# Kernel optimization log

Measured on AMD Instinct MI355X. Metric: run time of the kernel, lower is better.

## Reference

```python
import jax, jax.numpy as jnp
import numpy as np

IN_FEATURES = 1024
OUT_FEATURES = 128


def setup_inputs() -> dict:
    key = jax.random.key(0)
    k1, k2, k3, k4, k5 = jax.random.split(key, 5)
    B, T, E, D = 4, 4096, IN_FEATURES, OUT_FEATURES
    s_in = 1.0 / np.sqrt(E)
    s_d = 1.0 / np.sqrt(D)
    return {
        "x": jax.random.normal(k1, (B, T, E), dtype=jnp.float32),
        "Wk": jax.random.uniform(k2, (E, D), jnp.float32, -s_in, s_in),
        "Wq": jax.random.uniform(k3, (E, D), jnp.float32, -s_in, s_in),
        "Wv": jax.random.uniform(k4, (E, D), jnp.float32, -s_in, s_in),
        "Wp": jax.random.uniform(k5, (D, D), jnp.float32, -s_d, s_d),
    }


def reference(x, Wk, Wq, Wv, Wp):
    # x: [B, T, E]; projections stored as [in, out] (torch Linear transposed)
    B, T, E = x.shape
    D = Wk.shape[1]
    k = x @ Wk  # [B, T, D]
    q = x @ Wq
    v = x @ Wv
    scale = 1.0 / jnp.sqrt(jnp.asarray(D, x.dtype))
    attn = jnp.einsum("btd,bsd->bts", q, k) * scale  # [B, T, T]
    causal = jnp.tril(jnp.ones((T, T), dtype=bool))
    attn = jnp.where(causal, attn, -jnp.inf)
    attn = jax.nn.softmax(attn, axis=-1)
    out = jnp.einsum("bts,bsd->btd", attn, v)  # [B, T, D]
    return out @ Wp  # dropout p=0.0 -> identity
```

## Files before the change

kernel.cpp:

```cpp
#include <hip/hip_runtime.h>

#define E_DIM 1024
#define D_DIM 128
#define T_DIM 4096

typedef unsigned short u16;
typedef u16 u16x8 __attribute__((ext_vector_type(8)));
typedef u16 u16x4 __attribute__((ext_vector_type(4)));
typedef __bf16 bf16x8 __attribute__((ext_vector_type(8)));
typedef float f32x4 __attribute__((ext_vector_type(4)));

__device__ __forceinline__ u16 cvt_bf16(float f) {
    unsigned u = __float_as_uint(f);
    u += 0x7FFF + ((u >> 16) & 1);
    return (u16)(u >> 16);
}

__device__ __forceinline__ float bf2f(u16 v) {
    return __uint_as_float(((unsigned)v) << 16);
}

__device__ __forceinline__ f32x4 mfma16(u16x8 a, u16x8 b, f32x4 c) {
    return __builtin_amdgcn_mfma_f32_16x16x32_bf16(
        __builtin_bit_cast(bf16x8, a), __builtin_bit_cast(bf16x8, b), c, 0, 0, 0);
}

__device__ __forceinline__ void gld_lds16(const void* g, void* l) {
    __builtin_amdgcn_global_load_lds(
        (const __attribute__((address_space(1))) unsigned int*)g,
        (__attribute__((address_space(3))) unsigned int*)l, 16, 0, 0);
}

__global__ void prep_kernel(const float* __restrict__ Wk, const float* __restrict__ Wq,
                            const float* __restrict__ Wv, const float* __restrict__ Wp,
                            u16* __restrict__ Wqt, u16* __restrict__ Wkt,
                            u16* __restrict__ Wvt, u16* __restrict__ Wpt) {
    int tid = blockIdx.x * 256 + threadIdx.x;
    const int WT = 128 * 1024;
    if (tid < 3 * WT) {
        int w = tid / WT;
        int r = tid - w * WT;
        int n = r >> 10, k = r & 1023;
        const float* W = (w == 0) ? Wq : (w == 1) ? Wk : Wv;
        u16* Wt = (w == 0) ? Wqt : (w == 1) ? Wkt : Wvt;
        Wt[r] = cvt_bf16(W[k * 128 + n]);
    } else {
        int r = tid - 3 * WT;
        if (r < 128 * 128) {
            int n = r >> 7, k = r & 127;
            Wpt[r] = cvt_bf16(Wp[k * 128 + n]);
        }
    }
}

__global__ __launch_bounds__(256) void qkv_kernel(
        const float* __restrict__ x,
        const u16* __restrict__ Wqt, const u16* __restrict__ Wkt, const u16* __restrict__ Wvt,
        u16* __restrict__ qb, u16* __restrict__ kb, u16* __restrict__ vT) {
    __shared__ u16 Xs[64][40];
    __shared__ u16 Ws[3][128][40];

    const int t = threadIdx.x;
    const int w = t >> 6;
    const int lane = t & 63;
    const int lr = lane & 15;
    const int lg = lane >> 4;
    const int r0 = blockIdx.x * 64;

    f32x4 acc[24];
    #pragma unroll
    for (int i = 0; i < 24; ++i) acc[i] = f32x4{0.f, 0.f, 0.f, 0.f};

    const int xrow = t >> 2;
    const int xseg = t & 3;
    const int wn   = t >> 1;
    const int wh   = (t & 1) * 16;

    const float* xp0 = x + (size_t)(r0 + xrow) * E_DIM + xseg * 8;

    float4 a0 = *(const float4*)(xp0);
    float4 a1 = *(const float4*)(xp0 + 4);
    u16x8 wr[3][2];
    {
        const u16* w0 = Wqt + (size_t)wn * E_DIM + wh;
        const u16* w1 = Wkt + (size_t)wn * E_DIM + wh;
        const u16* w2 = Wvt + (size_t)wn * E_DIM + wh;
        wr[0][0] = *(const u16x8*)w0; wr[0][1] = *(const u16x8*)(w0 + 8);
        wr[1][0] = *(const u16x8*)w1; wr[1][1] = *(const u16x8*)(w1 + 8);
        wr[2][0] = *(const u16x8*)w2; wr[2][1] = *(const u16x8*)(w2 + 8);
    }

    for (int k0 = 0; k0 < E_DIM; k0 += 32) {
        u16x8 xv;
        xv[0] = cvt_bf16(a0.x); xv[1] = cvt_bf16(a0.y);
        xv[2] = cvt_bf16(a0.z); xv[3] = cvt_bf16(a0.w);
        xv[4] = cvt_bf16(a1.x); xv[5] = cvt_bf16(a1.y);
        xv[6] = cvt_bf16(a1.z); xv[7] = cvt_bf16(a1.w);
        *(u16x8*)&Xs[xrow][xseg * 8] = xv;
        #pragma unroll
        for (int j = 0; j < 3; ++j) {
            *(u16x8*)&Ws[j][wn][wh]     = wr[j][0];
            *(u16x8*)&Ws[j][wn][wh + 8] = wr[j][1];
        }
        __syncthreads();

        if (k0 + 32 < E_DIM) {
            const float* xp = xp0 + k0 + 32;
            a0 = *(const float4*)(xp);
            a1 = *(const float4*)(xp + 4);
            const u16* w0 = Wqt + (size_t)wn * E_DIM + k0 + 32 + wh;
            const u16* w1 = Wkt + (size_t)wn * E_DIM + k0 + 32 + wh;
            const u16* w2 = Wvt + (size_t)wn * E_DIM + k0 + 32 + wh;
            wr[0][0] = *(const u16x8*)w0; wr[0][1] = *(const u16x8*)(w0 + 8);
            wr[1][0] = *(const u16x8*)w1; wr[1][1] = *(const u16x8*)(w1 + 8);
            wr[2][0] = *(const u16x8*)w2; wr[2][1] = *(const u16x8*)(w2 + 8);
        }

        u16x8 av = *(u16x8*)&Xs[16 * w + lr][lg * 8];
        #pragma unroll
        for (int nt = 0; nt < 24; ++nt) {
            int j = nt >> 3;
            int n = (nt & 7) * 16 + lr;
            u16x8 bv = *(u16x8*)&Ws[j][n][lg * 8];
            acc[nt] = mfma16(av, bv, acc[nt]);
        }
        __syncthreads();
    }

    const int row0 = r0 + 16 * w + 4 * lg;
    const int bb = row0 >> 12;
    const int tt = row0 & 4095;
    #pragma unroll
    for (int nt = 0; nt < 24; ++nt) {
        int j = nt >> 3;
        int col = (nt & 7) * 16 + lr;
        if (j < 2) {
            u16* outb = (j == 0) ? qb : kb;
            #pragma unroll
            for (int reg = 0; reg < 4; ++reg)
                outb[(size_t)(row0 + reg) * D_DIM + col] = cvt_bf16(acc[nt][reg]);
        } else {
            u16x4 pv;
            #pragma unroll
            for (int reg = 0; reg < 4; ++reg) pv[reg] = cvt_bf16(acc[nt][reg]);
            *(u16x4*)&vT[((size_t)(bb * 128 + col)) * T_DIM + tt] = pv;
        }
    }
}

__global__ __launch_bounds__(512) void attn_kernel(
        const u16* __restrict__ qb, const u16* __restrict__ kb, const u16* __restrict__ vT,
        u16* __restrict__ Opart, float* __restrict__ ml, int SPLIT) {
    const int g = blockIdx.x;
    const int b = blockIdx.y;
    int i, c;
    if (SPLIT) {
        int k = 0;
        while (2 * (k + 1) * (k + 2) <= g) ++k;
        const int off = g - 2 * k * (k + 1);
        const int iband = off / (k + 1);
        c = off - iband * (k + 1);
        i = 4 * k + iband;
    } else { i = g; c = 0; }

    const int q0 = i * 128;
    const int kv_beg = c * 512;
    const int kv_end = SPLIT ? min(q0 + 128, kv_beg + 512) : (q0 + 128);
    const int slot = b * gridDim.x + g;

    __shared__ __align__(16) char smem[81920];

    const int t = threadIdx.x;
    const int w = t >> 6;
    const int lane = t & 63;
    const int lr = lane & 15;
    const int lg = lane >> 4;
    const size_t base = (size_t)b * T_DIM * D_DIM;

    u16x8 qf[4];
    {
        const u16* qp = qb + base + (size_t)(q0 + 16 * w + lr) * D_DIM + lg * 8;
        #pragma unroll
        for (int dk = 0; dk < 4; ++dk) qf[dk] = *(const u16x8*)(qp + dk * 32);
    }

    const char* kpb = (const char*)(kb + base);
    const char* vpb = (const char*)(vT + (size_t)b * D_DIM * T_DIM);
    const int key = (lr & 7) << 4;

    #define STAGE(S0, BUF) do {                                                   \
        char* kB_ = smem + (BUF) * 16384;                                         \
        char* vB_ = smem + 32768 + (BUF) * 16384;                                 \
        const int wbase_ = (t >> 6) * 1024;                                       \
        _Pragma("unroll")                                                         \
        for (int c2 = 0; c2 < 2; ++c2) {                                          \
            const int krow_ = c2 * 32 + (t >> 4);                                 \
            gld_lds16(kpb + (size_t)((S0) + krow_) * 256 +                        \
                      (((t & 15) * 16) ^ ((krow_ & 7) * 16)),                     \
                      kB_ + c2 * 8192 + wbase_);                                  \
            const int vrow_ = c2 * 64 + (t >> 3);                                 \
            gld_lds16(vpb + (size_t)vrow_ * (T_DIM * 2) + (size_t)(S0) * 2 +      \
                      (((t & 7) * 16) ^ ((vrow_ & 7) * 16)),                      \
                      vB_ + c2 * 8192 + wbase_);                                  \
        }                                                                         \
    } while (0)

    f32x4 oacc[8];
    #pragma unroll
    for (int n = 0; n < 8; ++n) oacc[n] = f32x4{0.f, 0.f, 0.f, 0.f};
    float m_run = -1e30f, l_run = 0.f;
    const float scale2 = 0.12752048520120164f;
    const int qrow = q0 + 16 * w + lr;

    STAGE(kv_beg, 0);
    asm volatile("s_waitcnt vmcnt(0)" ::: "memory");
    __syncthreads();

    int buf = 0;
    for (int s0 = kv_beg; s0 < kv_end; s0 += 64) {
        if (s0 + 64 < kv_end) STAGE(s0 + 64, buf ^ 1);

        char* kB  = smem + buf * 16384;
        char* vB  = smem + 32768 + buf * 16384;
        char* psB = smem + 65536 + w * 2048;

        f32x4 sacc[4];
        #pragma unroll
        for (int n = 0; n < 4; ++n) sacc[n] = f32x4{0.f, 0.f, 0.f, 0.f};
        __builtin_amdgcn_s_setprio(1);
        #pragma unroll
        for (int dk = 0; dk < 4; ++dk) {
            #pragma unroll
            for (int nt = 0; nt < 4; ++nt) {
                u16x8 kfr = *(u16x8*)(kB + (nt * 16 + lr) * 256 + ((dk * 64 + lg * 16) ^ key));
                sacc[nt] = mfma16(kfr, qf[dk], sacc[nt]);
            }
        }
        __builtin_amdgcn_s_setprio(0);

        float sv[4][4];
        const bool need_mask = (s0 + 63 > q0 + 16 * w);
        #pragma unroll
        for (int nt = 0; nt < 4; ++nt) {
            #pragma unroll
            for (int r = 0; r < 4; ++r) {
                float v = sacc[nt][r] * scale2;
                if (need_mask && (s0 + nt * 16 + 4 * lg + r) > qrow) v = -1e30f;
                sv[nt][r] = v;
            }
        }

        float tmax = sv[0][0];
        #pragma unroll
        for (int nt = 0; nt < 4; ++nt)
            #pragma unroll
            for (int r = 0; r < 4; ++r) tmax = fmaxf(tmax, sv[nt][r]);
        tmax = fmaxf(tmax, __shfl_xor(tmax, 16));
        tmax = fmaxf(tmax, __shfl_xor(tmax, 32));
        float m_new = fmaxf(m_run, tmax);
        float rsc = __builtin_amdgcn_exp2f(m_run - m_new);
        m_run = m_new;
        float tsum = 0.f;
        #pragma unroll
        for (int nt = 0; nt < 4; ++nt)
            #pragma unroll
            for (int r = 0; r < 4; ++r) {
                sv[nt][r] = __builtin_amdgcn_exp2f(sv[nt][r] - m_new);
                tsum += sv[nt][r];
            }
        tsum += __shfl_xor(tsum, 16);
        tsum += __shfl_xor(tsum, 32);
        l_run = l_run * rsc + tsum;

        #pragma unroll
        for (int nt = 0; nt < 8; ++nt)
            #pragma unroll
            for (int r = 0; r < 4; ++r) oacc[nt][r] *= rsc;

        #pragma unroll
        for (int nt = 0; nt < 4; ++nt) {
            u16x4 pv4;
            #pragma unroll
            for (int r = 0; r < 4; ++r) pv4[r] = cvt_bf16(sv[nt][r]);
            *(u16x4*)(psB + lr * 128 + ((nt * 32 + lg * 8) ^ key)) = pv4;
        }

        u16x8 pA0 = *(u16x8*)(psB + lr * 128 + ((lg * 16) ^ key));
        u16x8 pA1 = *(u16x8*)(psB + lr * 128 + ((64 + lg * 16) ^ key));

        __builtin_amdgcn_s_setprio(1);
        #pragma unroll
        for (int nt = 0; nt < 8; ++nt) {
            u16x8 bv0 = *(u16x8*)(vB + (nt * 16 + lr) * 128 + ((lg * 16) ^ key));
            oacc[nt] = mfma16(bv0, pA0, oacc[nt]);
            u16x8 bv1 = *(u16x8*)(vB + (nt * 16 + lr) * 128 + ((64 + lg * 16) ^ key));
            oacc[nt] = mfma16(bv1, pA1, oacc[nt]);
        }
        __builtin_amdgcn_s_setprio(0);

        asm volatile("s_waitcnt vmcnt(0)" ::: "memory");
        __syncthreads();
        buf ^= 1;
    }
    #undef STAGE

    if (lg == 0) {
        int row = 16 * w + lr;
        ml[(size_t)(slot * 128 + row) * 2]     = m_run;
        ml[(size_t)(slot * 128 + row) * 2 + 1] = l_run;
    }

    const float invl = 1.f / l_run;
    const int orw = 16 * w + lr;
    #pragma unroll
    for (int nt = 0; nt < 8; ++nt) {
        u16x4 ov;
        #pragma unroll
        for (int r = 0; r < 4; ++r) ov[r] = cvt_bf16(oacc[nt][r] * invl);
        *(u16x4*)(smem + orw * 256 + ((32 * nt + 8 * lg) ^ ((orw & 7) << 4))) = ov;
    }
    __syncthreads();
    u16* op = Opart + (size_t)slot * 16384;
    const int orow = t >> 2;
    const int oseg = t & 3;
    #pragma unroll
    for (int j = 0; j < 4; ++j) {
        u16x8 vv = *(u16x8*)(smem + orow * 256 + ((oseg * 64 + j * 16) ^ ((orow & 7) << 4)));
        *(u16x8*)(op + orow * 128 + oseg * 32 + j * 8) = vv;
    }
}

__global__ __launch_bounds__(256) void combine_kernel(
        const u16* __restrict__ Opart, const float* __restrict__ ml,
        const u16* __restrict__ Wpt, float* __restrict__ out,
        int SPLIT, int NSLOT) {
    const int io = blockIdx.x;
    const int b = blockIdx.y;
    const int i = io >> 1;
    const int half = io & 1;
    int NC, g0;
    if (SPLIT) {
        int k = i >> 2;
        NC = k + 1;
        g0 = 2 * k * (k + 1) + (i & 3) * (k + 1);
    } else { NC = 1; g0 = i; }
    const int slot0 = b * NSLOT + g0;

    __shared__ u16 Os[64][136];
    const int t = threadIdx.x;
    const int row = t >> 2, seg = (t & 3) * 32;
    const int row_in = half * 64 + row;

    float m_fin = -1e30f;
    for (int c = 0; c < NC; ++c)
        m_fin = fmaxf(m_fin, ml[(size_t)((slot0 + c) * 128 + row_in) * 2]);

    float acc[32];
    #pragma unroll
    for (int j = 0; j < 32; ++j) acc[j] = 0.f;
    float l_fin = 0.f;
    for (int c = 0; c < NC; ++c) {
        float mcv = ml[(size_t)((slot0 + c) * 128 + row_in) * 2];
        float lcv = ml[(size_t)((slot0 + c) * 128 + row_in) * 2 + 1];
        float wgt = __builtin_amdgcn_exp2f(mcv - m_fin) * lcv;
        l_fin += wgt;
        const u16* opc = Opart + (size_t)(slot0 + c) * 16384 + row_in * 128 + seg;
        #pragma unroll
        for (int j = 0; j < 4; ++j) {
            u16x8 v = *(const u16x8*)(opc + j * 8);
            #pragma unroll
            for (int e = 0; e < 8; ++e)
                acc[j * 8 + e] += bf2f(v[e]) * wgt;
        }
    }
    const float inv = 1.f / l_fin;

    #pragma unroll
    for (int j = 0; j < 4; ++j) {
        u16x8 ov;
        #pragma unroll
        for (int e = 0; e < 8; ++e) ov[e] = cvt_bf16(acc[j * 8 + e] * inv);
        *(u16x8*)&Os[row][seg + j * 8] = ov;
    }
    __syncthreads();

    const int w = t >> 6;
    const int lane = t & 63;
    const int lr = lane & 15;
    const int lg = lane >> 4;
    u16x8 af[4];
    #pragma unroll
    for (int dk = 0; dk < 4; ++dk)
        af[dk] = *(u16x8*)&Os[16 * w + lr][dk * 32 + lg * 8];
    float* op = out + ((size_t)b * T_DIM + io * 64) * D_DIM;
    #pragma unroll
    for (int nt = 0; nt < 8; ++nt) {
        f32x4 y = f32x4{0.f, 0.f, 0.f, 0.f};
        #pragma unroll
        for (int dk = 0; dk < 4; ++dk) {
            u16x8 bv = *(const u16x8*)&Wpt[(size_t)(nt * 16 + lr) * D_DIM + dk * 32 + lg * 8];
            y = mfma16(af[dk], bv, y);
        }
        #pragma unroll
        for (int r = 0; r < 4; ++r)
            op[(size_t)(16 * w + 4 * lg + r) * D_DIM + nt * 16 + lr] = y[r];
    }
}

extern "C" void kernel_launch(void* const* d_in, const int* in_sizes, int n_in,
                              void* d_out, int out_size, void* d_ws, size_t ws_size,
                              hipStream_t stream) {
    const float* x  = (const float*)d_in[0];
    const float* Wk = (const float*)d_in[1];
    const float* Wq = (const float*)d_in[2];
    const float* Wv = (const float*)d_in[3];
    const float* Wp = (const float*)d_in[4];
    float* out = (float*)d_out;

    char* ws = (char*)d_ws;
    u16* qb  = (u16*)(ws);
    u16* kb  = (u16*)(ws + 4194304);
    u16* vT  = (u16*)(ws + 8388608);
    u16* Wqt = (u16*)(ws + 12582912);
    u16* Wkt = (u16*)(ws + 12582912 + 262144);
    u16* Wvt = (u16*)(ws + 12582912 + 524288);
    u16* Wpt = (u16*)(ws + 12582912 + 786432);
    float* ml   = (float*)(ws + 13631488);
    u16* Opart  = (u16*)(ws + 14680064);

    const bool big = ws_size >= (size_t)36 * 1024 * 1024;
    const int SPLIT = big ? 1 : 0;
    const int GX = big ? 144 : 32;

    prep_kernel<<<1600, 256, 0, stream>>>(Wk, Wq, Wv, Wp, Wqt, Wkt, Wvt, Wpt);
    qkv_kernel<<<256, 256, 0, stream>>>(x, Wqt, Wkt, Wvt, qb, kb, vT);
    attn_kernel<<<dim3(GX, 4), 512, 0, stream>>>(qb, kb, vT, Opart, ml, SPLIT);
    combine_kernel<<<dim3(64, 4), 256, 0, stream>>>(Opart, ml, Wpt, out, SPLIT, GX);
}
```

Before: 107.9 us.

## Restructure QKV projection GEMM: split output columns, async weight staging, direct-register x

The QKV projection kernel now launches twice as many blocks, each covering 64 rows by 192 of the 384 fused output columns. Each wave computes a 32x96 sub-tile, so every weight fragment read from LDS feeds two MFMAs. Weights are double-buffered into LDS with direct global-to-LDS loads and an XOR-style swizzle. The x rows are loaded straight into registers and converted to bf16 there, which removes the x LDS round trip. The aim is more parallelism across CUs, fewer LDS reads per MFMA, and weight fetches overlapped with compute, at the cost of reading x twice (once per column group) and a vmcnt wait every iteration.

```diff
diff --git a/kernel.cpp b/kernel.cpp
--- a/kernel.cpp
+++ b/kernel.cpp
@@ -57,93 +57,107 @@
         const float* __restrict__ x,
         const u16* __restrict__ Wqt, const u16* __restrict__ Wkt, const u16* __restrict__ Wvt,
         u16* __restrict__ qb, u16* __restrict__ kb, u16* __restrict__ vT) {
-    __shared__ u16 Xs[64][40];
-    __shared__ u16 Ws[3][128][40];
+    __shared__ __align__(16) char smem[24576];
 
     const int t = threadIdx.x;
     const int w = t >> 6;
     const int lane = t & 63;
     const int lr = lane & 15;
     const int lg = lane >> 4;
-    const int r0 = blockIdx.x * 64;
-
-    f32x4 acc[24];
-    #pragma unroll
-    for (int i = 0; i < 24; ++i) acc[i] = f32x4{0.f, 0.f, 0.f, 0.f};
-
-    const int xrow = t >> 2;
-    const int xseg = t & 3;
-    const int wn   = t >> 1;
-    const int wh   = (t & 1) * 16;
-
-    const float* xp0 = x + (size_t)(r0 + xrow) * E_DIM + xseg * 8;
-
-    float4 a0 = *(const float4*)(xp0);
-    float4 a1 = *(const float4*)(xp0 + 4);
-    u16x8 wr[3][2];
-    {
-        const u16* w0 = Wqt + (size_t)wn * E_DIM + wh;
-        const u16* w1 = Wkt + (size_t)wn * E_DIM + wh;
-        const u16* w2 = Wvt + (size_t)wn * E_DIM + wh;
-        wr[0][0] = *(const u16x8*)w0; wr[0][1] = *(const u16x8*)(w0 + 8);
-        wr[1][0] = *(const u16x8*)w1; wr[1][1] = *(const u16x8*)(w1 + 8);
-        wr[2][0] = *(const u16x8*)w2; wr[2][1] = *(const u16x8*)(w2 + 8);
-    }
-
+    const int m = w & 1;
+    const int n = w >> 1;
+    const int rg = blockIdx.x >> 1;
+    const int cgrp = blockIdx.x & 1;
+    const int r0 = rg * 64;
+
+    #define STAGE_W(K0, BUF) do {                                                 \
+        char* wB_ = smem + (BUF) * 12288;                                         \
+        _Pragma("unroll")                                                         \
+        for (int c2 = 0; c2 < 3; ++c2) {                                          \
+            const int rl_ = c2 * 64 + (t >> 2);                                   \
+            const int gn_ = cgrp * 192 + rl_;                                     \
+            const u16* W_ = (gn_ < 128) ? Wqt : (gn_ < 256) ? Wkt : Wvt;          \
+            const int s_ = ((t & 3) - (rl_ >> 1)) & 3;                            \
+            gld_lds16(W_ + (size_t)(gn_ & 127) * E_DIM + (K0) + 8 * s_,           \
+                      wB_ + c2 * 4096 + t * 16);                                  \
+        }                                                                         \
+    } while (0)
+
+    const float* xp0 = x + (size_t)(r0 + 32 * m + lr) * E_DIM + lg * 8;
+    const float* xp1 = xp0 + 16 * E_DIM;
+
+    float4 xr[2][2];
+    #define XLOAD(K0) do {                                                        \
+        xr[0][0] = *(const float4*)(xp0 + (K0));                                  \
+        xr[0][1] = *(const float4*)(xp0 + (K0) + 4);                              \
+        xr[1][0] = *(const float4*)(xp1 + (K0));                                  \
+        xr[1][1] = *(const float4*)(xp1 + (K0) + 4);                              \
+    } while (0)
+
+    f32x4 acc[2][6];
+    #pragma unroll
+    for (int i = 0; i < 2; ++i)
+        #pragma unroll
+        for (int j = 0; j < 6; ++j) acc[i][j] = f32x4{0.f, 0.f, 0.f, 0.f};
+
+    XLOAD(0);
+    STAGE_W(0, 0);
+    asm volatile("s_waitcnt vmcnt(0)" ::: "memory");
+    __syncthreads();
+
+    int buf = 0;
     for (int k0 = 0; k0 < E_DIM; k0 += 32) {
-        u16x8 xv;
-        xv[0] = cvt_bf16(a0.x); xv[1] = cvt_bf16(a0.y);
-        xv[2] = cvt_bf16(a0.z); xv[3] = cvt_bf16(a0.w);
-        xv[4] = cvt_bf16(a1.x); xv[5] = cvt_bf16(a1.y);
-        xv[6] = cvt_bf16(a1.z); xv[7] = cvt_bf16(a1.w);
-        *(u16x8*)&Xs[xrow][xseg * 8] = xv;
-        #pragma unroll
-        for (int j = 0; j < 3; ++j) {
-            *(u16x8*)&Ws[j][wn][wh]     = wr[j][0];
-            *(u16x8*)&Ws[j][wn][wh + 8] = wr[j][1];
-        }
+        if (k0 + 32 < E_DIM) STAGE_W(k0 + 32, buf ^ 1);
+
+        u16x8 av[2];
+        #pragma unroll
+        for (int i = 0; i < 2; ++i) {
+            av[i][0] = cvt_bf16(xr[i][0].x); av[i][1] = cvt_bf16(xr[i][0].y);
+            av[i][2] = cvt_bf16(xr[i][0].z); av[i][3] = cvt_bf16(xr[i][0].w);
+            av[i][4] = cvt_bf16(xr[i][1].x); av[i][5] = cvt_bf16(xr[i][1].y);
+            av[i][6] = cvt_bf16(xr[i][1].z); av[i][7] = cvt_bf16(xr[i][1].w);
+        }
+        if (k0 + 32 < E_DIM) XLOAD(k0 + 32);
+
+        char* wB = smem + buf * 12288;
+        __builtin_amdgcn_s_setprio(1);
+        #pragma unroll
+        for (int nt = 0; nt < 6; ++nt) {
+            const int ln = n * 96 + nt * 16 + lr;
+            u16x8 bv = *(u16x8*)(wB + ln * 64 + (((lg + (ln >> 1)) & 3) << 4));
+            acc[0][nt] = mfma16(av[0], bv, acc[0][nt]);
+            acc[1][nt] = mfma16(av[1], bv, acc[1][nt]);
+        }
+        __builtin_amdgcn_s_setprio(0);
+
+        asm volatile("s_waitcnt vmcnt(0)" ::: "memory");
         __syncthreads();
-
-        if (k0 + 32 < E_DIM) {
-            const float* xp = xp0 + k0 + 32;
-            a0 = *(const float4*)(xp);
-            a1 = *(const float4*)(xp + 4);
-            const u16* w0 = Wqt + (size_t)wn * E_DIM + k0 + 32 + wh;
-            const u16* w1 = Wkt + (size_t)wn * E_DIM + k0 + 32 + wh;
-            const u16* w2 = Wvt + (size_t)wn * E_DIM + k0 + 32 + wh;
-            wr[0][0] = *(const u16x8*)w0; wr[0][1] = *(const u16x8*)(w0 + 8);
-            wr[1][0] = *(const u16x8*)w1; wr[1][1] = *(const u16x8*)(w1 + 8);
-            wr[2][0] = *(const u16x8*)w2; wr[2][1] = *(const u16x8*)(w2 + 8);
-        }
-
-        u16x8 av = *(u16x8*)&Xs[16 * w + lr][lg * 8];
-        #pragma unroll
-        for (int nt = 0; nt < 24; ++nt) {
-            int j = nt >> 3;
-            int n = (nt & 7) * 16 + lr;
-            u16x8 bv = *(u16x8*)&Ws[j][n][lg * 8];
-            acc[nt] = mfma16(av, bv, acc[nt]);
-        }
-        __syncthreads();
-    }
-
-    const int row0 = r0 + 16 * w + 4 * lg;
-    const int bb = row0 >> 12;
-    const int tt = row0 & 4095;
-    #pragma unroll
-    for (int nt = 0; nt < 24; ++nt) {
-        int j = nt >> 3;
-        int col = (nt & 7) * 16 + lr;
-        if (j < 2) {
-            u16* outb = (j == 0) ? qb : kb;
-            #pragma unroll
-            for (int reg = 0; reg < 4; ++reg)
-                outb[(size_t)(row0 + reg) * D_DIM + col] = cvt_bf16(acc[nt][reg]);
-        } else {
-            u16x4 pv;
-            #pragma unroll
-            for (int reg = 0; reg < 4; ++reg) pv[reg] = cvt_bf16(acc[nt][reg]);
-            *(u16x4*)&vT[((size_t)(bb * 128 + col)) * T_DIM + tt] = pv;
+        buf ^= 1;
+    }
+    #undef STAGE_W
+    #undef XLOAD
+
+    const int bb = r0 >> 12;
+    #pragma unroll
+    for (int i = 0; i < 2; ++i) {
+        const int row0 = r0 + 32 * m + 16 * i + 4 * lg;
+        const int tt0 = row0 & 4095;
+        #pragma unroll
+        for (int nt = 0; nt < 6; ++nt) {
+            const int col_g = cgrp * 192 + n * 96 + nt * 16 + lr;
+            const int j = col_g >> 7;
+            const int colw = col_g & 127;
+            if (j < 2) {
+                u16* outb = (j == 0) ? qb : kb;
+                #pragma unroll
+                for (int reg = 0; reg < 4; ++reg)
+                    outb[(size_t)(row0 + reg) * D_DIM + colw] = cvt_bf16(acc[i][nt][reg]);
+            } else {
+                u16x4 pv;
+                #pragma unroll
+                for (int reg = 0; reg < 4; ++reg) pv[reg] = cvt_bf16(acc[i][nt][reg]);
+                *(u16x4*)&vT[((size_t)(bb * 128 + colw)) * T_DIM + tt0] = pv;
+            }
         }
     }
 }
@@ -207,7 +221,7 @@
 
     f32x4 oacc[8];
     #pragma unroll
-    for (int n = 0; n < 8; ++n) oacc[n] = f32x4{0.f, 0.f, 0.f, 0.f};
+    for (int nn = 0; nn < 8; ++nn) oacc[nn] = f32x4{0.f, 0.f, 0.f, 0.f};
     float m_run = -1e30f, l_run = 0.f;
     const float scale2 = 0.12752048520120164f;
     const int qrow = q0 + 16 * w + lr;
@@ -226,7 +240,7 @@
 
         f32x4 sacc[4];
         #pragma unroll
-        for (int n = 0; n < 4; ++n) sacc[n] = f32x4{0.f, 0.f, 0.f, 0.f};
+        for (int nn = 0; nn < 4; ++nn) sacc[nn] = f32x4{0.f, 0.f, 0.f, 0.f};
         __builtin_amdgcn_s_setprio(1);
         #pragma unroll
         for (int dk = 0; dk < 4; ++dk) {
@@ -433,7 +447,7 @@
     const int GX = big ? 144 : 32;
 
     prep_kernel<<<1600, 256, 0, stream>>>(Wk, Wq, Wv, Wp, Wqt, Wkt, Wvt, Wpt);
-    qkv_kernel<<<256, 256, 0, stream>>>(x, Wqt, Wkt, Wvt, qb, kb, vT);
+    qkv_kernel<<<512, 256, 0, stream>>>(x, Wqt, Wkt, Wvt, qb, kb, vT);
     attn_kernel<<<dim3(GX, 4), 512, 0, stream>>>(qb, kb, vT, Opart, ml, SPLIT);
     combine_kernel<<<dim3(64, 4), 256, 0, stream>>>(Opart, ml, Wpt, out, SPLIT, GX);
 }
```

New measurement: 106.2 us. Within noise of the previous version (-1.5%).
